# Optimization experiments

Hardware: AMD Instinct MI355X
Metric: run time of the kernel (lower is better)

## Reference

```python
import jax, jax.numpy as jnp
import numpy as np

EPS = 0.1
P, C, T_MLP, C_MLP, B = 196, 768, 384, 3072, 64


def yat(x, W, b, alpha):
    # x: (..., in), W: (out, in), b: (out,), alpha: (1,)
    dot_nb = jnp.einsum('...i,oi->...o', x, W)          # no-bias dot (shared GEMM)
    dot = dot_nb + b
    w_norm_sq = jnp.sum(W * W, axis=1)                   # (out,)
    x_norm_sq = jnp.sum(x * x, axis=-1, keepdims=True)   # (..., 1)
    dist_sq = w_norm_sq + x_norm_sq - 2.0 * dot_nb
    out_f = W.shape[0]
    scale_base = out_f / np.log(out_f + 1.0)
    scale = jnp.sqrt(jnp.asarray(scale_base, x.dtype)) ** alpha[0]
    return scale * (dot * dot) / (dist_sq + EPS)


def setup_inputs() -> dict:
    key = jax.random.key(0)
    ks = jax.random.split(key, 7)
    x = jax.random.normal(ks[0], (B, P, C), dtype=jnp.float32)
    # token-mixing YAT: in=P, out=T_MLP
    tw = jax.random.normal(ks[1], (T_MLP, P), dtype=jnp.float32) / np.sqrt(P)
    tb = jnp.zeros((T_MLP,), jnp.float32)
    t_alpha = jnp.ones((1,), jnp.float32)
    # token-mixing linear: T_MLP -> P
    w2 = jax.random.uniform(ks[2], (P, T_MLP), jnp.float32, -1, 1) / np.sqrt(T_MLP)
    b2 = jax.random.uniform(ks[3], (P,), jnp.float32, -1, 1) / np.sqrt(T_MLP)
    # channel-mixing YAT: in=C, out=C_MLP
    cw = jax.random.normal(ks[4], (C_MLP, C), dtype=jnp.float32) / np.sqrt(C)
    cb = jnp.zeros((C_MLP,), jnp.float32)
    c_alpha = jnp.ones((1,), jnp.float32)
    # channel-mixing linear: C_MLP -> C
    w4 = jax.random.uniform(ks[5], (C, C_MLP), jnp.float32, -1, 1) / np.sqrt(C_MLP)
    b4 = jax.random.uniform(ks[6], (C,), jnp.float32, -1, 1) / np.sqrt(C_MLP)
    return {"x": x, "tw": tw, "tb": tb, "t_alpha": t_alpha, "w2": w2, "b2": b2,
            "cw": cw, "cb": cb, "c_alpha": c_alpha, "w4": w4, "b4": b4}


def reference(x, tw, tb, t_alpha, w2, b2, cw, cb, c_alpha, w4, b4):
    # Token mixing (operates over patch dim)
    shortcut = x
    xt = jnp.swapaxes(x, 1, 2)                 # (B, C, P)
    h = yat(xt, tw, tb, t_alpha)               # (B, C, T_MLP)
    h = jnp.einsum('bct,pt->bcp', h, w2) + b2  # (B, C, P)
    x = shortcut + jnp.swapaxes(h, 1, 2)
    # Channel mixing (operates over hidden dim)
    shortcut = x
    h = yat(x, cw, cb, c_alpha)                # (B, P, C_MLP)
    h = jnp.einsum('bpm,cm->bpc', h, w4) + b4  # (B, P, C)
    return shortcut + h
```

## Files before the change

### kernel.cpp

```cpp
#include <hip/hip_runtime.h>
#include <hip/hip_bf16.h>
#include <math.h>

#define B_   64
#define P_   196
#define PPAD 224
#define C_   768
#define TM_  384
#define CM_  3072
#define EPSY 0.1f

typedef unsigned short u16;
typedef __attribute__((ext_vector_type(8))) short bf16x8;
typedef __attribute__((ext_vector_type(4))) float f32x4;

__device__ __forceinline__ float bf2f(u16 v) {
    return __uint_as_float(((unsigned int)v) << 16);
}
__device__ __forceinline__ u16 f2bf(float f) {
    unsigned int u = __float_as_uint(f);
    unsigned int rounding = 0x7FFFu + ((u >> 16) & 1u);
    return (u16)((u + rounding) >> 16);
}

__device__ __forceinline__ void gl_lds16(const u16* g, u16* l) {
    __builtin_amdgcn_global_load_lds(
        (const __attribute__((address_space(1))) unsigned int*)g,
        (__attribute__((address_space(3))) unsigned int*)l,
        16, 0, 0);
}


__global__ __launch_bounds__(256) void k_prep_xT(const float* __restrict__ x,
                                                 u16* __restrict__ xT,
                                                 float* __restrict__ xn1) {
    __shared__ u16 tile[32][33];
    __shared__ float colsum[32];
    const int b = blockIdx.z, p0 = blockIdx.x * 32, c0 = blockIdx.y * 32;
    const int tx = threadIdx.x & 31, ty = threadIdx.x >> 5;
    if (threadIdx.x < 32) colsum[threadIdx.x] = 0.f;
    const float* xb = x + (size_t)b * P_ * C_;
    float s = 0.f;
    #pragma unroll
    for (int r = 0; r < 4; ++r) {
        int p = p0 + ty + r * 8;
        float v = (p < P_) ? xb[(size_t)p * C_ + c0 + tx] : 0.f;
        u16 h = f2bf(v);
        tile[ty + r * 8][tx] = h;
        float vb = bf2f(h);
        s = fmaf(vb, vb, s);
    }
    __syncthreads();
    u16* dst = xT + ((size_t)b * C_ + c0) * PPAD + p0;
    #pragma unroll
    for (int r = 0; r < 4; ++r) {
        int cl = ty + r * 8;
        dst[(size_t)cl * PPAD + tx] = tile[tx][cl];
    }
    atomicAdd(&colsum[tx], s);
    __syncthreads();
    if (threadIdx.x < 32)
        atomicAdd(&xn1[(size_t)b * C_ + c0 + threadIdx.x], colsum[threadIdx.x]);
}

__device__ __forceinline__ void pad_norm_body(const float* in, u16* outb, float* norm,
                                              int rows, int inlen, int outlen,
                                              int bid, int tid) {
    int wave = (bid * 256 + tid) >> 6;
    int lane = tid & 63;
    if (wave >= rows) return;
    const float* src = in + (size_t)wave * inlen;
    u16* dst = outb + (size_t)wave * outlen;
    float s = 0.f;
    for (int i = lane; i < outlen; i += 64) {
        float v = (i < inlen) ? src[i] : 0.f;
        u16 h = f2bf(v);
        dst[i] = h;
        float vv = bf2f(h);
        s = fmaf(vv, vv, s);
    }
    #pragma unroll
    for (int off = 32; off > 0; off >>= 1) s += __shfl_down(s, off, 64);
    if (lane == 0) norm[wave] = s;
}

__global__ __launch_bounds__(256) void k_prep_weights(
    const float* __restrict__ tw, u16* __restrict__ twb, float* __restrict__ twn,
    const float* __restrict__ cw, u16* __restrict__ cwb, float* __restrict__ cwn,
    const float* __restrict__ w2, u16* __restrict__ w2b,
    const float* __restrict__ w4, u16* __restrict__ w4b) {
    int bid = blockIdx.x, tid = threadIdx.x;
    if (bid < 96) {
        pad_norm_body(tw, twb, twn, TM_, P_, PPAD, bid, tid);
    } else if (bid < 864) {
        pad_norm_body(cw, cwb, cwn, CM_, C_, C_, bid - 96, tid);
    } else if (bid < 1248) {
        int idx = (bid - 864) * 256 + tid;
        int row = idx / TM_;
        w2b[idx] = (row < P_) ? f2bf(w2[(size_t)row * TM_ + (idx % TM_)]) : (u16)0;
    } else {
        int idx = (bid - 1248) * 256 + tid;
        float4 v = ((const float4*)w4)[idx];
        ushort4 o;
        o.x = f2bf(v.x); o.y = f2bf(v.y); o.z = f2bf(v.z); o.w = f2bf(v.w);
        ((ushort4*)w4b)[idx] = o;
    }
}

__device__ __forceinline__ void mfma_mainloop(
    const u16* __restrict__ A, const u16* __restrict__ B,
    int lda, int ldb, int kiters,
    f32x4 (&acc)[4][4], u16* As, u16* Bs) {
    const int t = threadIdx.x;
    const int w = t >> 6, l = t & 63;
    const int quad = l >> 4, l15 = l & 15;
    const int row0 = t >> 2, kc = (t & 3) * 8;

    const u16* pa0 = A + (size_t)row0 * lda + kc;
    const u16* pa1 = A + (size_t)(64 + row0) * lda + kc;
    const u16* pb0 = B + (size_t)row0 * ldb + kc;
    const u16* pb1 = B + (size_t)(64 + row0) * ldb + kc;

    u16* ldsA0 = As + w * 512;
    u16* ldsA1 = As + 2048 + w * 512;
    u16* ldsB0 = Bs + w * 512;
    u16* ldsB1 = Bs + 2048 + w * 512;

#define STAGE_(bsel, koff)                          \
    do {                                            \
        const int nb_ = (bsel) * 4096;              \
        gl_lds16(pa0 + (koff), ldsA0 + nb_);        \
        gl_lds16(pa1 + (koff), ldsA1 + nb_);        \
        gl_lds16(pb0 + (koff), ldsB0 + nb_);        \
        gl_lds16(pb1 + (koff), ldsB1 + nb_);        \
    } while (0)

    STAGE_(0, 0);
    if (kiters > 1) {
        STAGE_(1, 32);
        asm volatile("s_waitcnt vmcnt(4)" ::: "memory");
    } else {
        asm volatile("s_waitcnt vmcnt(0)" ::: "memory");
    }
    __builtin_amdgcn_s_barrier();

    int cur = 0;
    int koff = 64;
    for (int it = 0; it < kiters; ++it) {
        const u16* Aw = As + cur * 4096 + (w >> 1) * 2048;
        const u16* Bw = Bs + cur * 4096 + (w & 1) * 2048;
        bf16x8 af[4], bfr[4];
        #pragma unroll
        for (int i = 0; i < 4; ++i)
            af[i] = *(const bf16x8*)(Aw + ((i * 16 + l15) * 32 + quad * 8));
        #pragma unroll
        for (int j = 0; j < 4; ++j)
            bfr[j] = *(const bf16x8*)(Bw + ((j * 16 + l15) * 32 + quad * 8));
        asm volatile("s_waitcnt lgkmcnt(0)" ::: "memory");
        __builtin_amdgcn_sched_barrier(0);
        __builtin_amdgcn_s_barrier();
        const bool more2 = (it + 2 < kiters);
        if (more2) { STAGE_(cur, koff); koff += 32; }
        __builtin_amdgcn_s_setprio(1);
        #pragma unroll
        for (int i = 0; i < 4; ++i)
            #pragma unroll
            for (int j = 0; j < 4; ++j)
                acc[i][j] = __builtin_amdgcn_mfma_f32_16x16x32_bf16(af[i], bfr[j], acc[i][j], 0, 0, 0);
        __builtin_amdgcn_s_setprio(0);
        if (it + 1 < kiters) {
            if (more2) asm volatile("s_waitcnt vmcnt(4)" ::: "memory");
            else       asm volatile("s_waitcnt vmcnt(0)" ::: "memory");
            __builtin_amdgcn_s_barrier();
        }
        cur ^= 1;
    }
#undef STAGE_
}

#define MFMA_CORE(AP, BP, LDA, LDB, KITERS)                              \
    __shared__ u16 As[2 * 128 * 32];                                     \
    __shared__ u16 Bs[2 * 128 * 32];                                     \
    const int t = threadIdx.x;                                           \
    const int wid = t >> 6, lane = t & 63;                               \
    const int quad = lane >> 4, l15 = lane & 15;                         \
    f32x4 acc[4][4];                                                     \
    _Pragma("unroll")                                                    \
    for (int i = 0; i < 4; ++i)                                          \
        _Pragma("unroll")                                                \
        for (int j = 0; j < 4; ++j) acc[i][j] = (f32x4){0.f,0.f,0.f,0.f};\
    mfma_mainloop(AP, BP, LDA, LDB, KITERS, acc, As, Bs);                \
    const int rbase = m0 + (wid >> 1) * 64;                              \
    const int cbase = n0 + (wid & 1) * 64;

#define PH_MID()  do { __builtin_amdgcn_sched_barrier(0);                 \
    __builtin_amdgcn_s_barrier();                                         \
    asm volatile("s_waitcnt lgkmcnt(0)" ::: "memory");                    \
    __builtin_amdgcn_sched_barrier(0);                                    \
    __builtin_amdgcn_s_setprio(1); } while (0)
#define PH_END()  do { __builtin_amdgcn_s_setprio(0);                     \
    __builtin_amdgcn_sched_barrier(0);                                    \
    __builtin_amdgcn_s_barrier(); } while (0)
#define PH_END_VM(n) do { __builtin_amdgcn_s_setprio(0);                  \
    asm volatile("s_waitcnt vmcnt(" #n ")" ::: "memory");                 \
    __builtin_amdgcn_sched_barrier(0);                                    \
    __builtin_amdgcn_s_barrier(); } while (0)

#define DSA(d, half, Ar)                                                  \
    _Pragma("unroll")                                                     \
    for (int mi = 0; mi < 4; ++mi) {                                      \
        Ar[mi][0] = *(const bf16x8*)(aB0 + (d) * 16384 + ((half) * 4 + mi) * 1024); \
        Ar[mi][1] = *(const bf16x8*)(aB1 + (d) * 16384 + ((half) * 4 + mi) * 1024); \
    }
#define DSB(d, half, Br)                                                  \
    _Pragma("unroll")                                                     \
    for (int ni = 0; ni < 2; ++ni) {                                      \
        Br[ni][0] = *(const bf16x8*)(bB0 + (d) * 16384 + ((half) * 2 + ni) * 1024); \
        Br[ni][1] = *(const bf16x8*)(bB1 + (d) * 16384 + ((half) * 2 + ni) * 1024); \
    }
#define MMQ(mh, nh, Ar, Br)                                               \
    _Pragma("unroll")                                                     \
    for (int kk = 0; kk < 2; ++kk)                                        \
        _Pragma("unroll")                                                 \
        for (int mi = 0; mi < 4; ++mi)                                    \
            _Pragma("unroll")                                             \
            for (int ni = 0; ni < 2; ++ni)                                \
                acc[(mh) * 4 + mi][(nh) * 2 + ni] =                       \
                    __builtin_amdgcn_mfma_f32_16x16x32_bf16(              \
                        Ar[mi][kk], Br[ni][kk],                           \
                        acc[(mh) * 4 + mi][(nh) * 2 + ni], 0, 0, 0);
#define STG(isB, d, half, T)                                              \
    do {                                                                  \
        const u16* g_ = (isB) ? gB : gA;                                  \
        const int ld_ = (isB) ? ldb : lda;                                \
        u16* s_ = smem + ((isB) ? 32768 : 0) + (d) * 16384 + (half) * 4096 + sdst; \
        gl_lds16(g_ + (size_t)((half) * 64) * ld_ + (T) * 64, s_);        \
        gl_lds16(g_ + (size_t)((half) * 64 + 128) * ld_ + (T) * 64, s_ + 8192); \
    } while (0)

__device__ __forceinline__ void mfma8p_mainloop(
    const u16* __restrict__ A, const u16* __restrict__ B,
    int lda, int ldb, int ntiles,
    f32x4 (&acc)[8][4], u16* smem) {
    const int t = threadIdx.x;
    const int w = t >> 6, lane = t & 63;
    const int wr = w >> 2, wc = w & 3;
    const int quad = lane >> 4, l15 = lane & 15;

    const int srow = w * 8 + (lane >> 3);
    const int cofs = ((lane & 7) ^ (lane >> 3)) * 8;
    const int sdst = w * 512 + lane * 8;
    const u16* gA = A + (size_t)srow * lda + cofs;
    const u16* gB = B + (size_t)srow * ldb + cofs;

    const int q = (quad * 8) ^ ((l15 & 7) << 3);
    const u16* aB0 = smem + (wr * 128 + l15) * 64 + q;
    const u16* aB1 = smem + (wr * 128 + l15) * 64 + (q ^ 32);
    const u16* bB0 = smem + 32768 + (wc * 64 + l15) * 64 + q;
    const u16* bB1 = smem + 32768 + (wc * 64 + l15) * 64 + (q ^ 32);

    STG(0, 0, 0, 0); STG(0, 0, 1, 0); STG(1, 0, 0, 0); STG(1, 0, 1, 0);
    STG(0, 1, 0, 1); STG(1, 1, 1, 1); STG(0, 1, 1, 1);
    asm volatile("s_waitcnt vmcnt(6)" ::: "memory");
    __builtin_amdgcn_s_barrier();

    bf16x8 a[4][2], b[2][2], c[2][2];
    const int NI = ntiles >> 1;
    for (int i = 0; i < NI - 1; ++i) {
        const int T1t = 2 * i + 1, N0 = 2 * i + 2, N1 = 2 * i + 3;
        DSA(0, 0, a) DSB(0, 0, b)
        STG(1, 1, 0, T1t);
        PH_MID(); MMQ(0, 0, a, b) PH_END();
        DSB(0, 1, c)
        STG(0, 0, 0, N0);
        PH_MID(); MMQ(0, 1, a, c) PH_END();
        DSA(0, 1, a)
        STG(1, 0, 1, N0);
        PH_MID(); MMQ(1, 1, a, c) PH_END();
        STG(0, 0, 1, N0);
        PH_MID(); MMQ(1, 0, a, b) PH_END_VM(6);
        DSA(1, 0, a) DSB(1, 0, b)
        STG(1, 0, 0, N0);
        PH_MID(); MMQ(0, 0, a, b) PH_END();
        DSB(1, 1, c)
        STG(0, 1, 0, N1);
        PH_MID(); MMQ(0, 1, a, c) PH_END();
        DSA(1, 1, a)
        STG(1, 1, 1, N1);
        PH_MID(); MMQ(1, 1, a, c) PH_END();
        STG(0, 1, 1, N1);
        PH_MID(); MMQ(1, 0, a, b) PH_END_VM(6);
    }
    {
        const int T1t = 2 * NI - 1;
        DSA(0, 0, a) DSB(0, 0, b)
        STG(1, 1, 0, T1t);
        PH_MID(); MMQ(0, 0, a, b) PH_END();
        DSB(0, 1, c)
        PH_MID(); MMQ(0, 1, a, c) PH_END();
        DSA(0, 1, a)
        PH_MID(); MMQ(1, 1, a, c) PH_END();
        PH_MID(); MMQ(1, 0, a, b) PH_END_VM(0);
        DSA(1, 0, a) DSB(1, 0, b)
        PH_MID(); MMQ(0, 0, a, b) PH_END();
        DSB(1, 1, c)
        PH_MID(); MMQ(0, 1, a, c) PH_END();
        DSA(1, 1, a)
        PH_MID(); MMQ(1, 1, a, c) PH_END();
        PH_MID(); MMQ(1, 0, a, b) PH_END();
    }
}

__global__ __launch_bounds__(256) void k1_token_yat(
    const u16* __restrict__ xT, const u16* __restrict__ twb,
    const float* __restrict__ tb, const float* __restrict__ twn,
    const float* __restrict__ xn1, const float* __restrict__ alpha, float sb,
    u16* __restrict__ h1) {
    const int m0 = (blockIdx.x + blockIdx.y * 8) * 128;
    const int n0 = blockIdx.z * 128;
    MFMA_CORE(xT + (size_t)m0 * PPAD, twb + (size_t)n0 * PPAD, PPAD, PPAD, PPAD / 32)
    float scale = powf(sqrtf(sb), alpha[0]);
    #pragma unroll
    for (int i = 0; i < 4; ++i) {
        #pragma unroll
        for (int j = 0; j < 4; ++j) {
            int col = cbase + j * 16 + l15;
            float bn = tb[col], wnn = twn[col];
            #pragma unroll
            for (int reg = 0; reg < 4; ++reg) {
                int row = rbase + i * 16 + quad * 4 + reg;
                float dnb = acc[i][j][reg];
                float dot = dnb + bn;
                float dist = wnn + xn1[row] - 2.f * dnb;
                h1[(size_t)row * TM_ + col] = f2bf(scale * dot * dot / (dist + EPSY));
            }
        }
    }
}

__global__ __launch_bounds__(512, 2) void k3_chan_yat(
    const u16* __restrict__ x1b, const u16* __restrict__ cwb,
    const float* __restrict__ cb, const float* __restrict__ cwn,
    const float* __restrict__ xn2, const float* __restrict__ alpha, float sb,
    u16* __restrict__ h3) {
    __shared__ __align__(16) u16 smem[65536];
    const int mt = blockIdx.x + blockIdx.y * 8;
    if (mt >= (B_ * P_) / 256) return;
    const int m0 = mt * 256;
    const int n0 = blockIdx.z * 256;
    const int t = threadIdx.x;
    const int w = t >> 6, l = t & 63;
    const int wr = w >> 2, wc = w & 3;
    const int quad = l >> 4, l15 = l & 15;
    f32x4 acc[8][4];
    #pragma unroll
    for (int m = 0; m < 8; ++m)
        #pragma unroll
        for (int n = 0; n < 4; ++n) acc[m][n] = (f32x4){0.f, 0.f, 0.f, 0.f};
    mfma8p_mainloop(x1b + (size_t)m0 * C_, cwb + (size_t)n0 * C_,
                    C_, C_, C_ / 64, acc, smem);
    const int rbase = m0 + wr * 128;
    const int cbase = n0 + wc * 64;
    float scale = powf(sqrtf(sb), alpha[0]);
    #pragma unroll
    for (int m = 0; m < 8; ++m) {
        #pragma unroll
        for (int n = 0; n < 4; ++n) {
            int col = cbase + n * 16 + l15;
            float bn = cb[col], wnn = cwn[col];
            #pragma unroll
            for (int reg = 0; reg < 4; ++reg) {
                int row = rbase + m * 16 + quad * 4 + reg;
                float dnb = acc[m][n][reg];
                float dot = dnb + bn;
                float dist = wnn + xn2[row] - 2.f * dnb;
                h3[(size_t)row * CM_ + col] = f2bf(scale * dot * dot / (dist + EPSY));
            }
        }
    }
}

__global__ __launch_bounds__(256) void k2_token_out(
    const u16* __restrict__ w2b, const u16* __restrict__ h1,
    const float* __restrict__ b2, const float* __restrict__ x,
    float* __restrict__ xn2, u16* __restrict__ x1b) {
    const int m0 = blockIdx.x * 128, n0 = blockIdx.y * 128;
    const u16* Bz = h1 + (size_t)blockIdx.z * C_ * TM_;
    MFMA_CORE(w2b + (size_t)m0 * TM_, Bz + (size_t)n0 * TM_, TM_, TM_, TM_ / 32)
    const float* rz = x + (size_t)blockIdx.z * P_ * C_;
    u16* oz = x1b + (size_t)blockIdx.z * P_ * C_;
    float* xrow = xn2 + (size_t)blockIdx.z * P_;
    #pragma unroll
    for (int i = 0; i < 4; ++i) {
        #pragma unroll
        for (int reg = 0; reg < 4; ++reg) {
            int row = rbase + i * 16 + quad * 4 + reg;
            if (row < P_) {
                float bm = b2[row];
                float s = 0.f;
                #pragma unroll
                for (int j = 0; j < 4; ++j) {
                    int col = cbase + j * 16 + l15;
                    float v = acc[i][j][reg] + bm + rz[(size_t)row * C_ + col];
                    u16 h = f2bf(v);
                    oz[(size_t)row * C_ + col] = h;
                    float vb = bf2f(h);
                    s = fmaf(vb, vb, s);
                }
                s += __shfl_xor(s, 1, 64);
                s += __shfl_xor(s, 2, 64);
                s += __shfl_xor(s, 4, 64);
                s += __shfl_xor(s, 8, 64);
                if (l15 == 0) atomicAdd(&xrow[row], s);
            }
        }
    }
}

__global__ __launch_bounds__(512, 2) void k4_split(
    const u16* __restrict__ h3, const u16* __restrict__ w4b,
    u16* __restrict__ pbuf, int KK) {
    __shared__ __align__(16) u16 smem[65536];
    const int mt = blockIdx.x + blockIdx.y * 8;
    if (mt >= (B_ * P_) / 256) return;
    const int m0 = mt * 256;
    const int nz = blockIdx.z;
    const int n0 = (nz % 3) * 256;
    const int ks = nz / 3;
    const int kbase = ks * KK;
    const int t = threadIdx.x;
    const int w = t >> 6, l = t & 63;
    const int wr = w >> 2, wc = w & 3;
    const int quad = l >> 4, l15 = l & 15;
    f32x4 acc[8][4];
    #pragma unroll
    for (int m = 0; m < 8; ++m)
        #pragma unroll
        for (int n = 0; n < 4; ++n) acc[m][n] = (f32x4){0.f, 0.f, 0.f, 0.f};
    mfma8p_mainloop(h3 + (size_t)m0 * CM_ + kbase, w4b + (size_t)n0 * CM_ + kbase,
                    CM_, CM_, KK / 64, acc, smem);
    const int rbase = m0 + wr * 128;
    const int cbase = n0 + wc * 64;
    u16* dst = pbuf + (size_t)ks * ((size_t)B_ * P_ * C_);
    #pragma unroll
    for (int m = 0; m < 8; ++m) {
        #pragma unroll
        for (int n = 0; n < 4; ++n) {
            int col = cbase + n * 16 + l15;
            #pragma unroll
            for (int reg = 0; reg < 4; ++reg) {
                int row = rbase + m * 16 + quad * 4 + reg;
                dst[(size_t)row * C_ + col] = f2bf(acc[m][n][reg]);
            }
        }
    }
}

template <int NS>
__global__ __launch_bounds__(256) void k4_reduce(
    float* __restrict__ outp, const u16* __restrict__ pbuf,
    const u16* __restrict__ x1b, const float* __restrict__ b4) {
    int idx = blockIdx.x * 256 + threadIdx.x;
    int c = (idx * 4) % C_;
    ushort4 r = ((const ushort4*)x1b)[idx];
    float4 o;
    o.x = bf2f(r.x) + b4[c + 0];
    o.y = bf2f(r.y) + b4[c + 1];
    o.z = bf2f(r.z) + b4[c + 2];
    o.w = bf2f(r.w) + b4[c + 3];
    const size_t stride4 = (size_t)B_ * P_ * C_ / 4;
    #pragma unroll
    for (int s = 0; s < NS; ++s) {
        ushort4 p = ((const ushort4*)pbuf)[idx + s * stride4];
        o.x += bf2f(p.x); o.y += bf2f(p.y); o.z += bf2f(p.z); o.w += bf2f(p.w);
    }
    ((float4*)outp)[idx] = o;
}

__global__ __launch_bounds__(256) void gemm_k4_fb(
    const u16* __restrict__ A, const u16* __restrict__ Bmat,
    const float* __restrict__ biasN, const u16* __restrict__ resB,
    float* __restrict__ Fout) {
    __shared__ u16 As[128 * 32];
    __shared__ u16 Bs[64 * 32];
    const int t = threadIdx.x;
    const int wid = t >> 6, lane = t & 63;
    const int quad = lane >> 4, l15 = lane & 15;
    const int m0 = blockIdx.x * 128, n0 = blockIdx.y * 64;
    f32x4 acc[4][2];
    #pragma unroll
    for (int i = 0; i < 4; ++i)
        #pragma unroll
        for (int j = 0; j < 2; ++j) acc[i][j] = (f32x4){0.f, 0.f, 0.f, 0.f};
    const u16* Aw = As + (wid >> 1) * (64 * 32);
    const u16* Bw = Bs + (wid & 1) * (32 * 32);
    const int arow = t >> 2, akc = (t & 3) * 8;
    for (int k0 = 0; k0 < CM_; k0 += 32) {
        gl_lds16(A + (size_t)(m0 + arow) * CM_ + k0 + akc,      As + wid * 512);
        gl_lds16(A + (size_t)(m0 + 64 + arow) * CM_ + k0 + akc, As + 2048 + wid * 512);
        gl_lds16(Bmat + (size_t)(n0 + arow) * CM_ + k0 + akc,   Bs + wid * 512);
        __syncthreads();
        bf16x8 af[4], bfr[2];
        #pragma unroll
        for (int i = 0; i < 4; ++i)
            af[i] = *(const bf16x8*)(Aw + ((i * 16 + l15) * 32 + quad * 8));
        #pragma unroll
        for (int j = 0; j < 2; ++j)
            bfr[j] = *(const bf16x8*)(Bw + ((j * 16 + l15) * 32 + quad * 8));
        #pragma unroll
        for (int i = 0; i < 4; ++i)
            #pragma unroll
            for (int j = 0; j < 2; ++j)
                acc[i][j] = __builtin_amdgcn_mfma_f32_16x16x32_bf16(af[i], bfr[j], acc[i][j], 0, 0, 0);
        __syncthreads();
    }
    const int rbase = m0 + (wid >> 1) * 64;
    const int cbase = n0 + (wid & 1) * 32;
    #pragma unroll
    for (int i = 0; i < 4; ++i) {
        #pragma unroll
        for (int j = 0; j < 2; ++j) {
            int col = cbase + j * 16 + l15;
            float bn = biasN[col];
            #pragma unroll
            for (int reg = 0; reg < 4; ++reg) {
                int row = rbase + i * 16 + quad * 4 + reg;
                float v = acc[i][j][reg] + bn + bf2f(resB[(size_t)row * C_ + col]);
                Fout[(size_t)row * C_ + col] = v;
            }
        }
    }
}

extern "C" void kernel_launch(void* const* d_in, const int* in_sizes, int n_in,
                              void* d_out, int out_size, void* d_ws, size_t ws_size,
                              hipStream_t stream) {
    const float* x  = (const float*)d_in[0];
    const float* tw = (const float*)d_in[1];
    const float* tb = (const float*)d_in[2];
    const float* ta = (const float*)d_in[3];
    const float* w2 = (const float*)d_in[4];
    const float* b2 = (const float*)d_in[5];
    const float* cw = (const float*)d_in[6];
    const float* cb = (const float*)d_in[7];
    const float* ca = (const float*)d_in[8];
    const float* w4 = (const float*)d_in[9];
    const float* b4 = (const float*)d_in[10];
    float* out = (float*)d_out;

    char* ws = (char*)d_ws;
    u16* h1 = (u16*)ws;
    u16* xT = (u16*)(ws + 37748736);
    u16* h3 = (u16*)ws;
    size_t off = 77070336;
    u16* x1b = (u16*)(ws + off); off += (size_t)B_ * P_ * C_ * 2;
    u16* twb = (u16*)(ws + off); off += (size_t)TM_ * PPAD * 2;
    u16* w2b = (u16*)(ws + off); off += (size_t)256 * TM_ * 2;
    u16* cwb = (u16*)(ws + off); off += (size_t)CM_ * C_ * 2;
    u16* w4b = (u16*)(ws + off); off += (size_t)C_ * CM_ * 2;
    float* xn1 = (float*)(ws + off); off += (size_t)B_ * C_ * 4;
    float* xn2 = (float*)(ws + off); off += (size_t)B_ * P_ * 4;
    float* twn = (float*)(ws + off); off += (size_t)TM_ * 4;
    float* cwn = (float*)(ws + off); off += (size_t)CM_ * 4;
    u16* pbuf = (u16*)(ws + off);
    const size_t psz = (size_t)B_ * P_ * C_ * 2;

    int nsplit = 1;
    if (ws_size >= off + 4 * psz)      nsplit = 4;
    else if (ws_size >= off + 2 * psz) nsplit = 2;

    const float SBT = (float)TM_ / logf((float)TM_ + 1.0f);
    const float SBC = (float)CM_ / logf((float)CM_ + 1.0f);

    hipMemsetAsync(xn1, 0, (size_t)(B_ * C_ + B_ * P_) * 4, stream);
    k_prep_weights<<<3552, 256, 0, stream>>>(tw, twb, twn, cw, cwb, cwn,
                                             w2, w2b, w4, w4b);
    k_prep_xT<<<dim3(PPAD / 32, C_ / 32, B_), 256, 0, stream>>>(x, xT, xn1);

    k1_token_yat<<<dim3(8, 48, 3), 256, 0, stream>>>(
        xT, twb, tb, twn, xn1, ta, SBT, h1);

    k2_token_out<<<dim3(2, C_ / 128, B_), 256, 0, stream>>>(
        w2b, h1, b2, x, xn2, x1b);

    k3_chan_yat<<<dim3(8, 7, 12), 512, 0, stream>>>(
        x1b, cwb, cb, cwn, xn2, ca, SBC, h3);

    if (nsplit > 1) {
        k4_split<<<dim3(8, 7, 3 * nsplit), 512, 0, stream>>>(
            h3, w4b, pbuf, CM_ / nsplit);
        int n4 = B_ * P_ * C_ / 4;
        if (nsplit == 4)
            k4_reduce<4><<<(n4 + 255) / 256, 256, 0, stream>>>(out, pbuf, x1b, b4);
        else
            k4_reduce<2><<<(n4 + 255) / 256, 256, 0, stream>>>(out, pbuf, x1b, b4);
    } else {
        gemm_k4_fb<<<dim3(B_ * P_ / 128, C_ / 64), 256, 0, stream>>>(
            h3, w4b, b4, x1b, out);
    }
}
```

Baseline: 366.2 us.

## Use 16-wave blocks for channel GEMMs, halving per-wave accumulator tiles

The 256x256-tile GEMM mainloop used by the channel YAT and split-K output kernels now runs on 1024 threads (16 waves) instead of 512. Each wave owns a 64x64 output tile, half the previous 128x64, so accumulator registers are halved. The global-to-LDS staging is reworked so each thread issues one 16-byte load per half-tile with a new swizzle, and the wait counts are adjusted. The goal is more waves to hide latency and less register pressure. The cost is lower MFMA work per LDS read and more barrier overhead with 16 waves synchronising.

New measurement: 438.8 us. +19.8%, slower.

```diff
diff --git a/kernel.cpp b/kernel.cpp
--- a/kernel.cpp
+++ b/kernel.cpp
@@ -206,108 +206,107 @@
     __builtin_amdgcn_sched_barrier(0);                                    \
     __builtin_amdgcn_s_barrier(); } while (0)
 
-#define DSA(d, half, Ar)                                                  \
+#define STG16(isB, d, h, T)                                               \
+    gl_lds16(((isB) ? gB : gA) + (size_t)((h) * 128 + srow) *             \
+                 ((isB) ? ldb : lda) + (T) * 64 + scol,                   \
+             smem + ((isB) ? 32768 : 0) + (d) * 16384 + (h) * 8192 + t * 8)
+
+#define DSA16(d, mh, Ar)                                                  \
     _Pragma("unroll")                                                     \
-    for (int mi = 0; mi < 4; ++mi) {                                      \
-        Ar[mi][0] = *(const bf16x8*)(aB0 + (d) * 16384 + ((half) * 4 + mi) * 1024); \
-        Ar[mi][1] = *(const bf16x8*)(aB1 + (d) * 16384 + ((half) * 4 + mi) * 1024); \
-    }
-#define DSB(d, half, Br)                                                  \
+    for (int mi = 0; mi < 2; ++mi) {                                      \
+        Ar[mi][0] = *(const bf16x8*)(aB0 + (d) * 16384 + ((mh) * 2 + mi) * 1024); \
+        Ar[mi][1] = *(const bf16x8*)(aB1 + (d) * 16384 + ((mh) * 2 + mi) * 1024); \
+    }
+#define DSB16(d, nh, Br)                                                  \
     _Pragma("unroll")                                                     \
     for (int ni = 0; ni < 2; ++ni) {                                      \
-        Br[ni][0] = *(const bf16x8*)(bB0 + (d) * 16384 + ((half) * 2 + ni) * 1024); \
-        Br[ni][1] = *(const bf16x8*)(bB1 + (d) * 16384 + ((half) * 2 + ni) * 1024); \
-    }
-#define MMQ(mh, nh, Ar, Br)                                               \
+        Br[ni][0] = *(const bf16x8*)(bB0 + (d) * 16384 + ((nh) * 2 + ni) * 1024); \
+        Br[ni][1] = *(const bf16x8*)(bB1 + (d) * 16384 + ((nh) * 2 + ni) * 1024); \
+    }
+#define MMQ16(mh, nh, Br)                                                 \
     _Pragma("unroll")                                                     \
     for (int kk = 0; kk < 2; ++kk)                                        \
         _Pragma("unroll")                                                 \
-        for (int mi = 0; mi < 4; ++mi)                                    \
+        for (int mi = 0; mi < 2; ++mi)                                    \
             _Pragma("unroll")                                             \
             for (int ni = 0; ni < 2; ++ni)                                \
-                acc[(mh) * 4 + mi][(nh) * 2 + ni] =                       \
+                acc[(mh) * 2 + mi][(nh) * 2 + ni] =                       \
                     __builtin_amdgcn_mfma_f32_16x16x32_bf16(              \
-                        Ar[mi][kk], Br[ni][kk],                           \
-                        acc[(mh) * 4 + mi][(nh) * 2 + ni], 0, 0, 0);
-#define STG(isB, d, half, T)                                              \
-    do {                                                                  \
-        const u16* g_ = (isB) ? gB : gA;                                  \
-        const int ld_ = (isB) ? ldb : lda;                                \
-        u16* s_ = smem + ((isB) ? 32768 : 0) + (d) * 16384 + (half) * 4096 + sdst; \
-        gl_lds16(g_ + (size_t)((half) * 64) * ld_ + (T) * 64, s_);        \
-        gl_lds16(g_ + (size_t)((half) * 64 + 128) * ld_ + (T) * 64, s_ + 8192); \
-    } while (0)
-
-__device__ __forceinline__ void mfma8p_mainloop(
+                        a[mi][kk], Br[ni][kk],                            \
+                        acc[(mh) * 2 + mi][(nh) * 2 + ni], 0, 0, 0);
+
+__device__ __forceinline__ void mfma16w_mainloop(
     const u16* __restrict__ A, const u16* __restrict__ B,
     int lda, int ldb, int ntiles,
-    f32x4 (&acc)[8][4], u16* smem) {
+    f32x4 (&acc)[4][4], u16* smem) {
     const int t = threadIdx.x;
     const int w = t >> 6, lane = t & 63;
     const int wr = w >> 2, wc = w & 3;
     const int quad = lane >> 4, l15 = lane & 15;
 
-    const int srow = w * 8 + (lane >> 3);
-    const int cofs = ((lane & 7) ^ (lane >> 3)) * 8;
-    const int sdst = w * 512 + lane * 8;
-    const u16* gA = A + (size_t)srow * lda + cofs;
-    const u16* gB = B + (size_t)srow * ldb + cofs;
+    const int srow = t >> 3;
+    const int scol = (((t & 7) ^ (srow & 7)) << 3);
+    const u16* gA = A;
+    const u16* gB = B;
 
     const int q = (quad * 8) ^ ((l15 & 7) << 3);
-    const u16* aB0 = smem + (wr * 128 + l15) * 64 + q;
-    const u16* aB1 = smem + (wr * 128 + l15) * 64 + (q ^ 32);
+    const u16* aB0 = smem + (wr * 64 + l15) * 64 + q;
+    const u16* aB1 = smem + (wr * 64 + l15) * 64 + (q ^ 32);
     const u16* bB0 = smem + 32768 + (wc * 64 + l15) * 64 + q;
     const u16* bB1 = smem + 32768 + (wc * 64 + l15) * 64 + (q ^ 32);
 
-    STG(0, 0, 0, 0); STG(0, 0, 1, 0); STG(1, 0, 0, 0); STG(1, 0, 1, 0);
-    STG(0, 1, 0, 1); STG(1, 1, 1, 1); STG(0, 1, 1, 1);
-    asm volatile("s_waitcnt vmcnt(6)" ::: "memory");
+    STG16(1, 0, 0, 0); STG16(1, 0, 1, 0);
+    STG16(0, 0, 0, 0); STG16(0, 0, 1, 0);
+    STG16(1, 1, 0, 1); STG16(1, 1, 1, 1);
+    asm volatile("s_waitcnt vmcnt(2)" ::: "memory");
     __builtin_amdgcn_s_barrier();
 
-    bf16x8 a[4][2], b[2][2], c[2][2];
+    bf16x8 a[2][2], b[2][2], c[2][2];
     const int NI = ntiles >> 1;
     for (int i = 0; i < NI - 1; ++i) {
-        const int T1t = 2 * i + 1, N0 = 2 * i + 2, N1 = 2 * i + 3;
-        DSA(0, 0, a) DSB(0, 0, b)
-        STG(1, 1, 0, T1t);
-        PH_MID(); MMQ(0, 0, a, b) PH_END();
-        DSB(0, 1, c)
-        STG(0, 0, 0, N0);
-        PH_MID(); MMQ(0, 1, a, c) PH_END();
-        DSA(0, 1, a)
-        STG(1, 0, 1, N0);
-        PH_MID(); MMQ(1, 1, a, c) PH_END();
-        STG(0, 0, 1, N0);
-        PH_MID(); MMQ(1, 0, a, b) PH_END_VM(6);
-        DSA(1, 0, a) DSB(1, 0, b)
-        STG(1, 0, 0, N0);
-        PH_MID(); MMQ(0, 0, a, b) PH_END();
-        DSB(1, 1, c)
-        STG(0, 1, 0, N1);
-        PH_MID(); MMQ(0, 1, a, c) PH_END();
-        DSA(1, 1, a)
-        STG(1, 1, 1, N1);
-        PH_MID(); MMQ(1, 1, a, c) PH_END();
-        STG(0, 1, 1, N1);
-        PH_MID(); MMQ(1, 0, a, b) PH_END_VM(6);
+        const int T1 = 2 * i + 1, N0 = 2 * i + 2, N1 = 2 * i + 3;
+        DSA16(0, 0, a) DSB16(0, 0, b)
+        STG16(0, 1, 0, T1);
+        PH_MID(); MMQ16(0, 0, b) PH_END();
+        DSB16(0, 1, c)
+        STG16(0, 1, 1, T1);
+        PH_MID(); MMQ16(0, 1, c) PH_END();
+        DSA16(0, 1, a)
+        STG16(1, 0, 0, N0);
+        PH_MID(); MMQ16(1, 1, c) PH_END();
+        STG16(1, 0, 1, N0);
+        PH_MID(); MMQ16(1, 0, b) PH_END_VM(2);
+        DSA16(1, 0, a) DSB16(1, 0, b)
+        STG16(0, 0, 0, N0);
+        PH_MID(); MMQ16(0, 0, b) PH_END();
+        DSB16(1, 1, c)
+        STG16(0, 0, 1, N0);
+        PH_MID(); MMQ16(0, 1, c) PH_END();
+        DSA16(1, 1, a)
+        STG16(1, 1, 0, N1);
+        PH_MID(); MMQ16(1, 1, c) PH_END();
+        STG16(1, 1, 1, N1);
+        PH_MID(); MMQ16(1, 0, b) PH_END_VM(2);
     }
     {
-        const int T1t = 2 * NI - 1;
-        DSA(0, 0, a) DSB(0, 0, b)
-        STG(1, 1, 0, T1t);
-        PH_MID(); MMQ(0, 0, a, b) PH_END();
-        DSB(0, 1, c)
-        PH_MID(); MMQ(0, 1, a, c) PH_END();
-        DSA(0, 1, a)
-        PH_MID(); MMQ(1, 1, a, c) PH_END();
-        PH_MID(); MMQ(1, 0, a, b) PH_END_VM(0);
-        DSA(1, 0, a) DSB(1, 0, b)
-        PH_MID(); MMQ(0, 0, a, b) PH_END();
-        DSB(1, 1, c)
-        PH_MID(); MMQ(0, 1, a, c) PH_END();
-        DSA(1, 1, a)
-        PH_MID(); MMQ(1, 1, a, c) PH_END();
-        PH_MID(); MMQ(1, 0, a, b) PH_END();
+        const int T1 = ntiles - 1;
+        DSA16(0, 0, a) DSB16(0, 0, b)
+        STG16(0, 1, 0, T1);
+        PH_MID(); MMQ16(0, 0, b) PH_END();
+        DSB16(0, 1, c)
+        STG16(0, 1, 1, T1);
+        PH_MID(); MMQ16(0, 1, c) PH_END();
+        DSA16(0, 1, a)
+        PH_MID(); MMQ16(1, 1, c) PH_END();
+        PH_MID(); MMQ16(1, 0, b) PH_END_VM(0);
+        DSA16(1, 0, a) DSB16(1, 0, b)
+        PH_MID(); MMQ16(0, 0, b) PH_END();
+        DSB16(1, 1, c)
+        PH_MID(); MMQ16(0, 1, c) PH_END();
+        DSA16(1, 1, a)
+        PH_MID(); MMQ16(1, 1, c) PH_END();
+        PH_MID(); MMQ16(1, 0, b)
+        __builtin_amdgcn_s_setprio(0);
     }
 }
 
@@ -338,7 +337,7 @@
     }
 }
 
-__global__ __launch_bounds__(512, 2) void k3_chan_yat(
+__global__ __launch_bounds__(1024) void k3_chan_yat(
     const u16* __restrict__ x1b, const u16* __restrict__ cwb,
     const float* __restrict__ cb, const float* __restrict__ cwn,
     const float* __restrict__ xn2, const float* __restrict__ alpha, float sb,
@@ -352,18 +351,18 @@
     const int w = t >> 6, l = t & 63;
     const int wr = w >> 2, wc = w & 3;
     const int quad = l >> 4, l15 = l & 15;
-    f32x4 acc[8][4];
-    #pragma unroll
-    for (int m = 0; m < 8; ++m)
+    f32x4 acc[4][4];
+    #pragma unroll
+    for (int m = 0; m < 4; ++m)
         #pragma unroll
         for (int n = 0; n < 4; ++n) acc[m][n] = (f32x4){0.f, 0.f, 0.f, 0.f};
-    mfma8p_mainloop(x1b + (size_t)m0 * C_, cwb + (size_t)n0 * C_,
-                    C_, C_, C_ / 64, acc, smem);
-    const int rbase = m0 + wr * 128;
+    mfma16w_mainloop(x1b + (size_t)m0 * C_, cwb + (size_t)n0 * C_,
+                     C_, C_, C_ / 64, acc, smem);
+    const int rbase = m0 + wr * 64;
     const int cbase = n0 + wc * 64;
     float scale = powf(sqrtf(sb), alpha[0]);
     #pragma unroll
-    for (int m = 0; m < 8; ++m) {
+    for (int m = 0; m < 4; ++m) {
         #pragma unroll
         for (int n = 0; n < 4; ++n) {
             int col = cbase + n * 16 + l15;
@@ -417,7 +416,7 @@
     }
 }
 
-__global__ __launch_bounds__(512, 2) void k4_split(
+__global__ __launch_bounds__(1024) void k4_split(
     const u16* __restrict__ h3, const u16* __restrict__ w4b,
     u16* __restrict__ pbuf, int KK) {
     __shared__ __align__(16) u16 smem[65536];
@@ -432,18 +431,18 @@
     const int w = t >> 6, l = t & 63;
     const int wr = w >> 2, wc = w & 3;
     const int quad = l >> 4, l15 = l & 15;
-    f32x4 acc[8][4];
-    #pragma unroll
-    for (int m = 0; m < 8; ++m)
+    f32x4 acc[4][4];
+    #pragma unroll
+    for (int m = 0; m < 4; ++m)
         #pragma unroll
         for (int n = 0; n < 4; ++n) acc[m][n] = (f32x4){0.f, 0.f, 0.f, 0.f};
-    mfma8p_mainloop(h3 + (size_t)m0 * CM_ + kbase, w4b + (size_t)n0 * CM_ + kbase,
-                    CM_, CM_, KK / 64, acc, smem);
-    const int rbase = m0 + wr * 128;
+    mfma16w_mainloop(h3 + (size_t)m0 * CM_ + kbase, w4b + (size_t)n0 * CM_ + kbase,
+                     CM_, CM_, KK / 64, acc, smem);
+    const int rbase = m0 + wr * 64;
     const int cbase = n0 + wc * 64;
     u16* dst = pbuf + (size_t)ks * ((size_t)B_ * P_ * C_);
     #pragma unroll
-    for (int m = 0; m < 8; ++m) {
+    for (int m = 0; m < 4; ++m) {
         #pragma unroll
         for (int n = 0; n < 4; ++n) {
             int col = cbase + n * 16 + l15;
@@ -583,11 +582,11 @@
     k2_token_out<<<dim3(2, C_ / 128, B_), 256, 0, stream>>>(
         w2b, h1, b2, x, xn2, x1b);
 
-    k3_chan_yat<<<dim3(8, 7, 12), 512, 0, stream>>>(
+    k3_chan_yat<<<dim3(8, 7, 12), 1024, 0, stream>>>(
         x1b, cwb, cb, cwn, xn2, ca, SBC, h3);
 
     if (nsplit > 1) {
-        k4_split<<<dim3(8, 7, 3 * nsplit), 512, 0, stream>>>(
+        k4_split<<<dim3(8, 7, 3 * nsplit), 1024, 0, stream>>>(
             h3, w4b, pbuf, CM_ / nsplit);
         int n4 = B_ * P_ * C_ / 4;
         if (nsplit == 4)
```
